# Kernel optimization log

Measured on AMD Instinct MI355X. Metric: run time of the kernel, lower is better.

The kernel has to match this reference:

```python
import jax, jax.numpy as jnp
import numpy as np

N = 16384
C = 4        # in_channels
K = 16       # neighbors
H = 64       # mlp width


def setup_inputs() -> dict:
    key = jax.random.key(0)
    k0, k1, k2, k3, k4 = jax.random.split(key, 5)
    x = jax.random.normal(k0, (N, C), dtype=jnp.float32)
    # nn.Linear(2C, 64) and nn.Linear(64, 64): weight [out, in], bias [out]
    W1 = jax.random.normal(k1, (H, 2 * C), dtype=jnp.float32) * (1.0 / np.sqrt(2 * C))
    b1 = jax.random.normal(k2, (H,), dtype=jnp.float32) * 0.01
    W2 = jax.random.normal(k3, (H, H), dtype=jnp.float32) * (1.0 / np.sqrt(H))
    b2 = jax.random.normal(k4, (H,), dtype=jnp.float32) * 0.01
    return {"x": x, "W1": W1, "b1": b1, "W2": W2, "b2": b2}


def reference(x, W1, b1, W2, b2):
    # x: [N, C] single point cloud (torch code unsqueezes batch dim 0)
    xs = jax.lax.stop_gradient(x)  # knn indices computed under no_grad
    # pairwise = -||xi - xj||^2 = 2*xi.xj - ||xi||^2 - ||xj||^2
    xx = jnp.sum(xs * xs, axis=1)                      # [N]
    pairwise = 2.0 * (xs @ xs.T) - xx[:, None] - xx[None, :]  # [N, N]
    _, idx = jax.lax.top_k(pairwise, K)                # [N, K] (self included, dist 0 is max)
    neigh = x[idx]                                     # [N, K, C] gather
    center = jnp.broadcast_to(x[:, None, :], (x.shape[0], K, C))
    edge = jnp.concatenate([neigh - center, center], axis=-1)  # [N, K, 2C]
    h = jax.nn.relu(jnp.einsum('nkc,hc->nkh', edge, W1) + b1)
    h = jax.nn.relu(jnp.einsum('nkh,gh->nkg', h, W2) + b2)     # [N, K, H]
    out = jnp.mean(h, axis=1)                          # [N, H]
    return out[None]                                   # [1, N, H] matches torch output
```

## Files before the change

kernel.cpp:

```cpp
#include <hip/hip_runtime.h>
#include <math.h>

#define N_PTS 16384
#define K_NBR 16
#define H_DIM 64
#define TS    512
#define CAP   144

typedef unsigned long long u64;
typedef float v2f __attribute__((ext_vector_type(2)));

__device__ __forceinline__ int prefix_lt(u64 m) {
    return __builtin_amdgcn_mbcnt_hi((unsigned)(m >> 32),
           __builtin_amdgcn_mbcnt_lo((unsigned)m, 0));
}
__device__ __forceinline__ u64 mkkey(unsigned vbits, unsigned idx) {
    unsigned of = vbits ^ (unsigned)(((int)vbits >> 31) | 0x80000000);
    return ((u64)of << 32) | (unsigned)(~idx);
}
__device__ __forceinline__ unsigned keyidx(u64 k) { return ~(unsigned)k; }

__device__ __forceinline__ float readlane_f(float v, int l) {
    return __uint_as_float(__builtin_amdgcn_readlane(__float_as_uint(v), l));
}

__device__ __forceinline__ float wave_sort_f32(float v, int lane) {
#pragma unroll
    for (int k = 2; k <= 64; k <<= 1) {
#pragma unroll
        for (int j = k >> 1; j > 0; j >>= 1) {
            float o = __shfl_xor(v, j, 64);
            bool keep_min = (((lane & k) == 0) == ((lane & j) == 0));
            v = keep_min ? fminf(v, o) : fmaxf(v, o);
        }
    }
    return v;
}
__device__ __forceinline__ u64 wave_sort_u64(u64 v, int lane) {
#pragma unroll
    for (int k = 2; k <= 64; k <<= 1) {
#pragma unroll
        for (int j = k >> 1; j > 0; j >>= 1) {
            u64 o = __shfl_xor((unsigned long long)v, j, 64);
            bool keep_min = (((lane & k) == 0) == ((lane & j) == 0));
            u64 mn = (v < o) ? v : o;
            u64 mx = (v < o) ? o : v;
            v = keep_min ? mn : mx;
        }
    }
    return v;
}

__device__ __forceinline__ int wave_compact(uint2* buf, int cnt, float* tau,
                                            int lane) {
    float lm = -INFINITY;
    for (int s = lane; s < cnt; s += 64)
        lm = fmaxf(lm, __uint_as_float(buf[s].x));
    const float tv = readlane_f(wave_sort_f32(lm, lane), 48);
    int nc = 0;
    for (int s0 = 0; s0 < cnt; s0 += 64) {
        const int s = s0 + lane;
        uint2 e = make_uint2(0u, 0u);
        bool keep = false;
        if (s < cnt) { e = buf[s]; keep = (__uint_as_float(e.x) >= tv); }
        const u64 km = __ballot(keep);
        if (keep) buf[nc + prefix_lt(km)] = e;
        nc += (int)__popcll(km);
    }
    *tau = tv;
    return nc;
}

__global__ __launch_bounds__(256) void xx_kernel(const float4* __restrict__ x4,
                                                 float* __restrict__ xx) {
    int i = blockIdx.x * 256 + threadIdx.x;
    float4 v = x4[i];
    {
#pragma clang fp contract(off)
        float s0 = v.x * v.x;
        float s1 = v.y * v.y;
        float s2 = v.z * v.z;
        float s3 = v.w * v.w;
        xx[i] = ((s0 + s1) + s2) + s3;
    }
}

__global__ __launch_bounds__(256, 8) void knn_kernel(
        const float4* __restrict__ x4,
        const float* __restrict__ xx,
        int* __restrict__ knn) {
    __shared__ float xsc[4][TS];
    __shared__ float nxxs[TS];
    __shared__ uint2 buf[8][CAP];
    const int lane = threadIdx.x & 63;
    const int wave = threadIdx.x >> 6;
    const int row0 = blockIdx.x * 8 + wave * 2;

    float4 y[2]; float nxxi[2];
    uint2* bufr[2];
#pragma unroll
    for (int r = 0; r < 2; ++r) {
        const float4 t0 = x4[row0 + r];
        y[r] = make_float4(2.0f * t0.x, 2.0f * t0.y, 2.0f * t0.z, 2.0f * t0.w);
        nxxi[r] = -xx[row0 + r];
        bufr[r] = &buf[wave * 2 + r][0];
    }
    float tau[2]; int cnt[2];

    auto pair_p = [&](int e, int r) -> v2f {
        const v2f ax = *(const v2f*)&xsc[0][e];
        const v2f ay = *(const v2f*)&xsc[1][e];
        const v2f az = *(const v2f*)&xsc[2][e];
        const v2f aw = *(const v2f*)&xsc[3][e];
        const v2f nx = *(const v2f*)&nxxs[e];
        v2f acc = nx + (v2f){nxxi[r], nxxi[r]};
        acc = __builtin_elementwise_fma(ax, (v2f){y[r].x, y[r].x}, acc);
        acc = __builtin_elementwise_fma(ay, (v2f){y[r].y, y[r].y}, acc);
        acc = __builtin_elementwise_fma(az, (v2f){y[r].z, y[r].z}, acc);
        acc = __builtin_elementwise_fma(aw, (v2f){y[r].w, y[r].w}, acc);
        return acc;
    };

    for (int i = threadIdx.x; i < TS; i += 256) {
        const float4 v = x4[i];
        xsc[0][i] = v.x; xsc[1][i] = v.y; xsc[2][i] = v.z; xsc[3][i] = v.w;
        nxxs[i] = -xx[i];
    }
    __syncthreads();

    {
        const int e = 2 * lane;
#pragma unroll
        for (int r = 0; r < 2; ++r) {
            const v2f pp = pair_p(e, r);
            const float mx = fmaxf(pp.x, pp.y);
            tau[r] = readlane_f(wave_sort_f32(mx, lane), 48);
            const u64 ma = __ballot(pp.x >= tau[r]);
            const u64 mb = __ballot(pp.y >= tau[r]);
            const int ca = (int)__popcll(ma);
            if (pp.x >= tau[r])
                bufr[r][prefix_lt(ma)] =
                    make_uint2(__float_as_uint(pp.x), (unsigned)e);
            if (pp.y >= tau[r])
                bufr[r][ca + prefix_lt(mb)] =
                    make_uint2(__float_as_uint(pp.y), (unsigned)(e + 1));
            cnt[r] = ca + (int)__popcll(mb);
        }
    }

    auto do_iter = [&](int cbase) {
        const int e = (cbase & (TS - 1)) + 2 * lane;
        v2f pp[2]; u64 mm[2];
#pragma unroll
        for (int r = 0; r < 2; ++r) {
            pp[r] = pair_p(e, r);
            mm[r] = __ballot(fmaxf(pp[r].x, pp[r].y) > tau[r]);
        }
        if (mm[0] | mm[1]) {
#pragma unroll
            for (int r = 0; r < 2; ++r) {
                if (mm[r]) {
                    u64 ma = __ballot(pp[r].x > tau[r]);
                    u64 mb = __ballot(pp[r].y > tau[r]);
                    int add = (int)__popcll(ma) + (int)__popcll(mb);
                    if (cnt[r] + add > CAP) {
                        cnt[r] = wave_compact(bufr[r], cnt[r], &tau[r], lane);
                        ma = __ballot(pp[r].x > tau[r]);
                        mb = __ballot(pp[r].y > tau[r]);
                        add = (int)__popcll(ma) + (int)__popcll(mb);
                    }
                    const int ca = (int)__popcll(ma);
                    if (pp[r].x > tau[r])
                        bufr[r][cnt[r] + prefix_lt(ma)] =
                            make_uint2(__float_as_uint(pp[r].x),
                                       (unsigned)(cbase + 2 * lane));
                    if (pp[r].y > tau[r])
                        bufr[r][cnt[r] + ca + prefix_lt(mb)] =
                            make_uint2(__float_as_uint(pp[r].y),
                                       (unsigned)(cbase + 2 * lane + 1));
                    cnt[r] += add;
                }
            }
        }
    };

#pragma unroll
    for (int j = 1; j < TS / 128; ++j) do_iter(j * 128);

    for (int t = 1; t < N_PTS / TS; ++t) {
        const int base = t * TS;
        __syncthreads();
        for (int i = threadIdx.x; i < TS; i += 256) {
            const float4 v = x4[base + i];
            xsc[0][i] = v.x; xsc[1][i] = v.y; xsc[2][i] = v.z; xsc[3][i] = v.w;
            nxxs[i] = -xx[base + i];
        }
        __syncthreads();
#pragma unroll
        for (int j = 0; j < TS / 128; ++j) do_iter(base + j * 128);
    }

#pragma unroll
    for (int r = 0; r < 2; ++r) {
        const int c2 = wave_compact(bufr[r], cnt[r], &tau[r], lane);
        u64 key = 0;
        if (lane < c2) {
            const uint2 e = bufr[r][lane];
            key = mkkey(e.x, e.y);
        }
        key = wave_sort_u64(key, lane);
        if (lane >= 48)
            knn[(row0 + r) * K_NBR + (lane - 48)] = (int)keyidx(key);
    }
}

__global__ __launch_bounds__(256, 2) void mlp_kernel(
        const float4* __restrict__ x4,
        const int* __restrict__ knn,
        const float4* __restrict__ W2f4,
        const float* __restrict__ W1,
        const float* __restrict__ b1,
        const float* __restrict__ b2,
        float* __restrict__ out) {
    __shared__ __align__(16) float4 w2s[16][64];
    __shared__ __align__(16) float  h1s[4][32][68];
    __shared__ __align__(16) float4 xjs[4][32];
    const int lane = threadIdx.x & 63;
    const int wave = threadIdx.x >> 6;
    const int kq   = lane >> 4;
    const int gp   = lane & 15;
    const int p0   = (blockIdx.x * 4 + wave) * 2;

    for (int q = threadIdx.x; q < 1024; q += 256)
        w2s[q & 15][q >> 4] = W2f4[q];
    __syncthreads();

    float w1r[8];
#pragma unroll
    for (int c = 0; c < 8; ++c) w1r[c] = W1[lane * 8 + c];
    const float b1r = b1[lane];
    float b2r[4];
#pragma unroll
    for (int gq = 0; gq < 4; ++gq) b2r[gq] = b2[gq * 16 + gp];

    if (lane < 32) {
        const int pp = lane >> 4;
        const int nb = knn[(p0 + pp) * K_NBR + (lane & 15)];
        xjs[wave][lane] = x4[nb];
    }

#pragma unroll
    for (int pp = 0; pp < 2; ++pp) {
        const float4 xi = x4[p0 + pp];
        float hb = b1r;
        hb = fmaf(w1r[4] - w1r[0], xi.x, hb);
        hb = fmaf(w1r[5] - w1r[1], xi.y, hb);
        hb = fmaf(w1r[6] - w1r[2], xi.z, hb);
        hb = fmaf(w1r[7] - w1r[3], xi.w, hb);
#pragma unroll
        for (int k = 0; k < K_NBR; ++k) {
            const float4 xj = xjs[wave][pp * 16 + k];
            float h = hb;
            h = fmaf(w1r[0], xj.x, h);
            h = fmaf(w1r[1], xj.y, h);
            h = fmaf(w1r[2], xj.z, h);
            h = fmaf(w1r[3], xj.w, h);
            h1s[wave][pp * 16 + k][lane] = fmaxf(h, 0.0f);
        }
    }

    v2f acc[2][4][4];
#pragma unroll
    for (int pp = 0; pp < 2; ++pp)
#pragma unroll
        for (int kk = 0; kk < 4; ++kk)
#pragma unroll
            for (int gq = 0; gq < 4; ++gq)
                acc[pp][kk][gq] = (v2f){b2r[gq], 0.0f};

#pragma unroll
    for (int h4 = 0; h4 < 16; ++h4) {
        float4 w4[4];
#pragma unroll
        for (int gq = 0; gq < 4; ++gq) w4[gq] = w2s[h4][gq * 16 + gp];
#pragma unroll
        for (int pp = 0; pp < 2; ++pp) {
#pragma unroll
            for (int kk = 0; kk < 4; ++kk) {
                const float4 hv =
                    *(const float4*)&h1s[wave][pp * 16 + kq * 4 + kk][h4 * 4];
#pragma unroll
                for (int gq = 0; gq < 4; ++gq) {
                    acc[pp][kk][gq] = __builtin_elementwise_fma(
                        (v2f){hv.x, hv.y}, (v2f){w4[gq].x, w4[gq].y},
                        acc[pp][kk][gq]);
                    acc[pp][kk][gq] = __builtin_elementwise_fma(
                        (v2f){hv.z, hv.w}, (v2f){w4[gq].z, w4[gq].w},
                        acc[pp][kk][gq]);
                }
            }
        }
    }

#pragma unroll
    for (int pp = 0; pp < 2; ++pp) {
        float s[4];
#pragma unroll
        for (int gq = 0; gq < 4; ++gq) {
            s[gq] = 0.0f;
#pragma unroll
            for (int kk = 0; kk < 4; ++kk) {
                const float v = acc[pp][kk][gq].x + acc[pp][kk][gq].y;
                s[gq] += fmaxf(v, 0.0f);
            }
        }
#pragma unroll
        for (int off = 16; off <= 32; off <<= 1)
#pragma unroll
            for (int gq = 0; gq < 4; ++gq)
                s[gq] += __shfl_xor(s[gq], off, 64);

        out[(p0 + pp) * H_DIM + kq * 16 + gp] = s[kq] * (1.0f / 16.0f);
    }
}

extern "C" void kernel_launch(void* const* d_in, const int* in_sizes, int n_in,
                              void* d_out, int out_size, void* d_ws, size_t ws_size,
                              hipStream_t stream) {
    (void)in_sizes; (void)n_in; (void)out_size; (void)ws_size;
    const float* x  = (const float*)d_in[0];
    const float* W1 = (const float*)d_in[1];
    const float* b1 = (const float*)d_in[2];
    const float* W2 = (const float*)d_in[3];
    const float* b2 = (const float*)d_in[4];
    float* out = (float*)d_out;

    float* xx  = (float*)d_ws;
    int*   knn = (int*)((char*)d_ws + N_PTS * sizeof(float));

    const float4* x4 = (const float4*)x;

    xx_kernel <<<N_PTS / 256, 256, 0, stream>>>(x4, xx);
    knn_kernel<<<N_PTS / 8,   256, 0, stream>>>(x4, xx, knn);
    mlp_kernel<<<N_PTS / 8,   256, 0, stream>>>(
        x4, knn, (const float4*)W2, W1, b1, b2, out);
}
```

Measured before the change: 214.9 us.

## Double-buffer kNN tiles with register prefetch from a precomputed planar layout

A prep kernel now writes x as structure-of-arrays planes plus a negated squared-norm plane, so each tile can be fetched with coalesced float4 loads. The kNN kernel keeps two LDS buffers and prefetches the next tile into registers while the current tile is scored, which removes one barrier per tile and hides global load latency. It also drops the per-row constant -xx_i term, since a shift shared by a whole row does not change its top-k order. The catch is that LDS per block roughly grows by half, which can lower resident blocks per CU, and scores now differ slightly in rounding, which could flip near-ties.

```diff
diff --git a/kernel.cpp b/kernel.cpp
--- a/kernel.cpp
+++ b/kernel.cpp
@@ -71,89 +71,90 @@
     return nc;
 }
 
-__global__ __launch_bounds__(256) void xx_kernel(const float4* __restrict__ x4,
-                                                 float* __restrict__ xx) {
+__global__ __launch_bounds__(256) void plane_kernel(const float4* __restrict__ x4,
+                                                    float* __restrict__ pl) {
     int i = blockIdx.x * 256 + threadIdx.x;
     float4 v = x4[i];
+    float nxx;
     {
 #pragma clang fp contract(off)
         float s0 = v.x * v.x;
         float s1 = v.y * v.y;
         float s2 = v.z * v.z;
         float s3 = v.w * v.w;
-        xx[i] = ((s0 + s1) + s2) + s3;
-    }
+        nxx = -(((s0 + s1) + s2) + s3);
+    }
+    pl[0 * N_PTS + i] = v.x;
+    pl[1 * N_PTS + i] = v.y;
+    pl[2 * N_PTS + i] = v.z;
+    pl[3 * N_PTS + i] = v.w;
+    pl[4 * N_PTS + i] = nxx;
 }
 
 __global__ __launch_bounds__(256, 8) void knn_kernel(
         const float4* __restrict__ x4,
-        const float* __restrict__ xx,
+        const float* __restrict__ pl,
         int* __restrict__ knn) {
-    __shared__ float xsc[4][TS];
-    __shared__ float nxxs[TS];
+    __shared__ __align__(16) float xsc[2][5][TS];
     __shared__ uint2 buf[8][CAP];
     const int lane = threadIdx.x & 63;
     const int wave = threadIdx.x >> 6;
     const int row0 = blockIdx.x * 8 + wave * 2;
-
-    float4 y[2]; float nxxi[2];
-    uint2* bufr[2];
+    const int NT = N_PTS / TS;
+
+    float4 y[2]; uint2* bufr[2];
 #pragma unroll
     for (int r = 0; r < 2; ++r) {
         const float4 t0 = x4[row0 + r];
         y[r] = make_float4(2.0f * t0.x, 2.0f * t0.y, 2.0f * t0.z, 2.0f * t0.w);
-        nxxi[r] = -xx[row0 + r];
         bufr[r] = &buf[wave * 2 + r][0];
     }
     float tau[2]; int cnt[2];
 
-    auto pair_p = [&](int e, int r) -> v2f {
-        const v2f ax = *(const v2f*)&xsc[0][e];
-        const v2f ay = *(const v2f*)&xsc[1][e];
-        const v2f az = *(const v2f*)&xsc[2][e];
-        const v2f aw = *(const v2f*)&xsc[3][e];
-        const v2f nx = *(const v2f*)&nxxs[e];
-        v2f acc = nx + (v2f){nxxi[r], nxxi[r]};
-        acc = __builtin_elementwise_fma(ax, (v2f){y[r].x, y[r].x}, acc);
+    float4 st[3];
+    auto issue = [&](int t) {
+        const int base = t * TS;
+#pragma unroll
+        for (int j = 0; j < 3; ++j) {
+            const int q = threadIdx.x + j * 256;
+            if (q < 640) {
+                const int c = q >> 7;
+                const int i = (q & 127) << 2;
+                st[j] = *(const float4*)&pl[c * N_PTS + base + i];
+            }
+        }
+    };
+    auto commit = [&](int b) {
+#pragma unroll
+        for (int j = 0; j < 3; ++j) {
+            const int q = threadIdx.x + j * 256;
+            if (q < 640) {
+                const int c = q >> 7;
+                const int i = (q & 127) << 2;
+                *(float4*)&xsc[b][c][i] = st[j];
+            }
+        }
+    };
+
+    auto pair_p = [&](int b, int e, int r) -> v2f {
+        const v2f ax = *(const v2f*)&xsc[b][0][e];
+        const v2f ay = *(const v2f*)&xsc[b][1][e];
+        const v2f az = *(const v2f*)&xsc[b][2][e];
+        const v2f aw = *(const v2f*)&xsc[b][3][e];
+        const v2f nx = *(const v2f*)&xsc[b][4][e];
+        v2f acc = __builtin_elementwise_fma(ax, (v2f){y[r].x, y[r].x}, nx);
         acc = __builtin_elementwise_fma(ay, (v2f){y[r].y, y[r].y}, acc);
         acc = __builtin_elementwise_fma(az, (v2f){y[r].z, y[r].z}, acc);
         acc = __builtin_elementwise_fma(aw, (v2f){y[r].w, y[r].w}, acc);
         return acc;
     };
 
-    for (int i = threadIdx.x; i < TS; i += 256) {
-        const float4 v = x4[i];
-        xsc[0][i] = v.x; xsc[1][i] = v.y; xsc[2][i] = v.z; xsc[3][i] = v.w;
-        nxxs[i] = -xx[i];
-    }
-    __syncthreads();
-
-    {
-        const int e = 2 * lane;
-#pragma unroll
-        for (int r = 0; r < 2; ++r) {
-            const v2f pp = pair_p(e, r);
-            const float mx = fmaxf(pp.x, pp.y);
-            tau[r] = readlane_f(wave_sort_f32(mx, lane), 48);
-            const u64 ma = __ballot(pp.x >= tau[r]);
-            const u64 mb = __ballot(pp.y >= tau[r]);
-            const int ca = (int)__popcll(ma);
-            if (pp.x >= tau[r])
-                bufr[r][prefix_lt(ma)] =
-                    make_uint2(__float_as_uint(pp.x), (unsigned)e);
-            if (pp.y >= tau[r])
-                bufr[r][ca + prefix_lt(mb)] =
-                    make_uint2(__float_as_uint(pp.y), (unsigned)(e + 1));
-            cnt[r] = ca + (int)__popcll(mb);
-        }
-    }
-
-    auto do_iter = [&](int cbase) {
+    auto do_iter = [&](int b, int cbase) {
         const int e = (cbase & (TS - 1)) + 2 * lane;
         v2f pp[2]; u64 mm[2];
 #pragma unroll
         for (int r = 0; r < 2; ++r) {
-            pp[r] = pair_p(e, r);
+            pp[r] = pair_p(b, e, r);
             mm[r] = __ballot(fmaxf(pp[r].x, pp[r].y) > tau[r]);
         }
         if (mm[0] | mm[1]) {
@@ -184,20 +185,39 @@
         }
     };
 
-#pragma unroll
-    for (int j = 1; j < TS / 128; ++j) do_iter(j * 128);
-
-    for (int t = 1; t < N_PTS / TS; ++t) {
-        const int base = t * TS;
+    issue(0); commit(0);
+    __syncthreads();
+    issue(1);
+
+    {
+        const int e = 2 * lane;
+#pragma unroll
+        for (int r = 0; r < 2; ++r) {
+            const v2f pp = pair_p(0, e, r);
+            const float mx = fmaxf(pp.x, pp.y);
+            tau[r] = readlane_f(wave_sort_f32(mx, lane), 48);
+            const u64 ma = __ballot(pp.x >= tau[r]);
+            const u64 mb = __ballot(pp.y >= tau[r]);
+            const int ca = (int)__popcll(ma);
+            if (pp.x >= tau[r])
+                bufr[r][prefix_lt(ma)] =
+                    make_uint2(__float_as_uint(pp.x), (unsigned)e);
+            if (pp.y >= tau[r])
+                bufr[r][ca + prefix_lt(mb)] =
+                    make_uint2(__float_as_uint(pp.y), (unsigned)(e + 1));
+            cnt[r] = ca + (int)__popcll(mb);
+        }
+    }
+#pragma unroll
+    for (int j = 1; j < TS / 128; ++j) do_iter(0, j * 128);
+
+    for (int t = 1; t < NT; ++t) {
+        const int b = t & 1;
+        commit(b);
         __syncthreads();
-        for (int i = threadIdx.x; i < TS; i += 256) {
-            const float4 v = x4[base + i];
-            xsc[0][i] = v.x; xsc[1][i] = v.y; xsc[2][i] = v.z; xsc[3][i] = v.w;
-            nxxs[i] = -xx[base + i];
-        }
-        __syncthreads();
-#pragma unroll
-        for (int j = 0; j < TS / 128; ++j) do_iter(base + j * 128);
+        if (t + 1 < NT) issue(t + 1);
+#pragma unroll
+        for (int j = 0; j < TS / 128; ++j) do_iter(b, t * TS + j * 128);
     }
 
 #pragma unroll
@@ -335,13 +355,13 @@
     const float* b2 = (const float*)d_in[4];
     float* out = (float*)d_out;
 
-    float* xx  = (float*)d_ws;
-    int*   knn = (int*)((char*)d_ws + N_PTS * sizeof(float));
+    float* pl  = (float*)d_ws;
+    int*   knn = (int*)((char*)d_ws + 5 * N_PTS * sizeof(float));
 
     const float4* x4 = (const float4*)x;
 
-    xx_kernel <<<N_PTS / 256, 256, 0, stream>>>(x4, xx);
-    knn_kernel<<<N_PTS / 8,   256, 0, stream>>>(x4, xx, knn);
-    mlp_kernel<<<N_PTS / 8,   256, 0, stream>>>(
+    plane_kernel<<<N_PTS / 256, 256, 0, stream>>>(x4, pl);
+    knn_kernel  <<<N_PTS / 8,   256, 0, stream>>>(x4, pl, knn);
+    mlp_kernel  <<<N_PTS / 8,   256, 0, stream>>>(
         x4, knn, (const float4*)W2, W1, b1, b2, out);
 }
```

New measurement: 316.8 us. +47.4%, slower.
